# Kernel tuning notes

Measured on AMD Instinct MI355X. Metric: run time of the kernel, lower is better.

Reference implementation:

```python
import jax, jax.numpy as jnp
import numpy as np

N, S = 65536, 2048        # dense points, sampled centres
D1, D2 = 64, 256          # skip-feature dim, centre-embedding dim
MLP = [256, 128]          # conv1x1 channel stack
BN_EPS = 1e-5             # flax BatchNorm default
INTERP_EPS = 1e-8


def setup_inputs() -> dict:
    key = jax.random.key(0)
    ks = jax.random.split(key, 6)
    inp = {
        "xyz1": jax.random.normal(ks[0], (3, N), jnp.float32),
        "xyz2": jax.random.normal(ks[1], (3, S), jnp.float32),
        "points1": jax.random.normal(ks[2], (D1, N), jnp.float32),
        "points2": jax.random.normal(ks[3], (D2, S), jnp.float32),
    }
    c_in = D1 + D2
    for i, c_out in enumerate(MLP):
        inp[f"w{i}"] = jax.random.normal(ks[4 + i], (c_in, c_out), jnp.float32) / np.float32(np.sqrt(c_in))
        inp[f"b{i}"] = jnp.zeros((c_out,), jnp.float32)
        inp[f"scale{i}"] = jnp.ones((c_out,), jnp.float32)
        inp[f"bias{i}"] = jnp.zeros((c_out,), jnp.float32)
        inp[f"mean{i}"] = jnp.zeros((c_out,), jnp.float32)   # BN running mean
        inp[f"var{i}"] = jnp.ones((c_out,), jnp.float32)     # BN running var
        c_in = c_out
    return inp


def reference(xyz1, xyz2, points1, points2,
              w0, b0, scale0, bias0, mean0, var0,
              w1, b1, scale1, bias1, mean1, var1):
    x1 = xyz1.T            # [N, 3]
    x2 = xyz2.T            # [S, 3]
    p2 = points2.T         # [S, D2]

    # squared pairwise distances [N, S]
    dists = (jnp.sum(x1 * x1, -1, keepdims=True)
             + jnp.sum(x2 * x2, -1)[None, :]
             - 2.0 * (x1 @ x2.T))

    # 3 nearest neighbours (smallest dist) per dense point
    neg_d3, idx = jax.lax.top_k(-dists, 3)      # [N, 3]
    d3 = -neg_d3
    recip = 1.0 / (d3 + INTERP_EPS)
    w = recip / jnp.sum(recip, axis=1, keepdims=True)   # [N, 3]

    # inverse-distance-weighted interpolation: [N, D2]
    interp = jnp.einsum('nkd,nk->nd', p2[idx], w)

    new = jnp.concatenate([points1.T, interp], axis=-1)  # [N, D1+D2]

    # conv1x1 (== dense) + BN (inference, running stats) + ReLU stack
    for W, b, s, bb, m, v in ((w0, b0, scale0, bias0, mean0, var0),
                              (w1, b1, scale1, bias1, mean1, var1)):
        y = new @ W + b
        y = (y - m) * (s / jnp.sqrt(v + BN_EPS)) + bb
        new = jax.nn.relu(y)

    return new.T           # [MLP[-1], N]
```

## Files before the change

### kernel.cpp

```cpp
#include <hip/hip_runtime.h>
#include <math.h>

#define NPTS 65536
#define NS   2048
#define C2   256
#define C3   128

#define WS_XYZ2P   0
#define WS_P2T     32768
#define WS_W0F     1081344
#define WS_W1F     1245184
#define WS_AB0     1310720
#define WS_AB1     1312768
#define WS_KIDX    1313792
#define WS_KW      2100224

typedef __attribute__((ext_vector_type(8))) short bf16x8;
typedef __attribute__((ext_vector_type(4))) float f32x4;

__device__ __forceinline__ unsigned short f2bf(float f) {
  unsigned u = __builtin_bit_cast(unsigned, f);
  u = (u + 0x7FFFu + ((u >> 16) & 1u)) >> 16;
  return (unsigned short)u;
}
__device__ __forceinline__ float bf2f(unsigned h) {
  return __builtin_bit_cast(float, h << 16);
}

__global__ __launch_bounds__(256) void pnfp_prep(
    const float* __restrict__ points2,
    const float* __restrict__ w0, const float* __restrict__ b0,
    const float* __restrict__ scale0, const float* __restrict__ bias0,
    const float* __restrict__ mean0, const float* __restrict__ var0,
    const float* __restrict__ w1, const float* __restrict__ b1,
    const float* __restrict__ scale1, const float* __restrict__ bias1,
    const float* __restrict__ mean1, const float* __restrict__ var1,
    unsigned char* __restrict__ ws)
{
  __shared__ float tile[64][65];
  const int tid = threadIdx.x;

  if (blockIdx.x < 128) {
    const int st = blockIdx.x & 31;
    const int dt = blockIdx.x >> 5;
#pragma unroll
    for (int it = 0; it < 16; ++it) {
      int j = it * 256 + tid;
      int d = j >> 6, s = j & 63;
      tile[d][s] = points2[(dt * 64 + d) * NS + st * 64 + s];
    }
    __syncthreads();
    unsigned short* p2t = (unsigned short*)(ws + WS_P2T);
#pragma unroll
    for (int it = 0; it < 16; ++it) {
      int j = it * 256 + tid;
      int s = j >> 6, d = j & 63;
      p2t[(st * 64 + s) * 256 + dt * 64 + d] = f2bf(tile[d][s]);
    }
    return;
  }

  int gid = (blockIdx.x - 128) * 256 + tid;
  if (gid < 81920) {
    int i = gid & 7, l = (gid >> 3) & 63, c = (gid >> 9) & 15, ks = gid >> 13;
    int k = ks * 32 + (l >> 4) * 8 + i;
    int col = c * 16 + (l & 15);
    ((unsigned short*)(ws + WS_W0F))[gid] = f2bf(w0[k * C2 + col]);
    return;
  }
  gid -= 81920;
  if (gid < 32768) {
    int i = gid & 7, l = (gid >> 3) & 63, c = (gid >> 9) & 7, ks = gid >> 12;
    int k = ks * 32 + (l >> 4) * 8 + i;
    int col = c * 16 + (l & 15);
    ((unsigned short*)(ws + WS_W1F))[gid] = f2bf(w1[k * C3 + col]);
    return;
  }
  gid -= 32768;
  if (gid < 256) {
    float a = scale0[gid] / sqrtf(var0[gid] + 1e-5f);
    float bb = (b0[gid] - mean0[gid]) * a + bias0[gid];
    float* ab = (float*)(ws + WS_AB0);
    ab[gid] = a; ab[256 + gid] = bb;
    return;
  }
  gid -= 256;
  if (gid < 128) {
    float a = scale1[gid] / sqrtf(var1[gid] + 1e-5f);
    float bb = (b1[gid] - mean1[gid]) * a + bias1[gid];
    float* ab = (float*)(ws + WS_AB1);
    ab[gid] = a; ab[128 + gid] = bb;
  }
}

__global__ __launch_bounds__(256) void pnfp_knn(
    const float* __restrict__ xyz1, const float* __restrict__ xyz2,
    unsigned char* __restrict__ ws)
{
  __shared__ float4 cs[2056];
  for (int j = threadIdx.x; j < NS; j += 256) {
    float x = xyz2[j], y = xyz2[NS + j], z = xyz2[2 * NS + j];
    float sc;
    {
#pragma clang fp contract(off)
      sc = (x * x + y * y) + z * z;
    }
    cs[j + (j >> 8)] = make_float4(x, y, z, sc);
  }
  __syncthreads();

  const int tid = threadIdx.x;
  const int rank = tid & 7;
  const int set = tid >> 3;
  const int nb = blockIdx.x * 128 + set * 4;

  float px[4], py[4], pz[4], ps[4];
#pragma unroll
  for (int p = 0; p < 4; ++p) {
    int n = nb + p;
    px[p] = xyz1[n]; py[p] = xyz1[NPTS + n]; pz[p] = xyz1[2 * NPTS + n];
    {
#pragma clang fp contract(off)
      ps[p] = (px[p] * px[p] + py[p] * py[p]) + pz[p] * pz[p];
    }
  }

  float D0[4], D1[4], D2[4];
  int I0[4], I1[4], I2[4];
#pragma unroll
  for (int p = 0; p < 4; ++p) {
    D0[p] = 1e30f; D1[p] = 1e30f; D2[p] = 1e30f;
    I0[p] = 0; I1[p] = 0; I2[p] = 0;
  }

  const float4* cq = cs + rank * 257;
  const int sbase = rank << 8;
#pragma unroll 4
  for (int t = 0; t < 256; ++t) {
    const float4 c = cq[t];
    const int s = sbase + t;
#pragma unroll
    for (int p = 0; p < 4; ++p) {
      float dot = fmaf(pz[p], c.z, fmaf(py[p], c.y, px[p] * c.x));
      float d = (ps[p] + c.w) - 2.0f * dot;
      const bool c2 = d < D2[p], c1 = d < D1[p], c0 = d < D0[p];
      I2[p] = c2 ? (c1 ? I1[p] : s) : I2[p];
      I1[p] = c1 ? (c0 ? I0[p] : s) : I1[p];
      I0[p] = c0 ? s : I0[p];
      float n1 = __builtin_amdgcn_fmed3f(D0[p], D1[p], d);
      float n2 = __builtin_amdgcn_fmed3f(D1[p], D2[p], d);
      D0[p] = fminf(D0[p], d);
      D1[p] = n1; D2[p] = n2;
    }
  }

#pragma unroll
  for (int p = 0; p < 4; ++p) {
#pragma unroll
    for (int m = 1; m <= 4; m <<= 1) {
      float e0 = __shfl_xor(D0[p], m), e1 = __shfl_xor(D1[p], m), e2 = __shfl_xor(D2[p], m);
      int  j0 = __shfl_xor(I0[p], m), j1 = __shfl_xor(I1[p], m), j2 = __shfl_xor(I2[p], m);
      bool t0 = e0 < D0[p];
      float r0 = t0 ? e0 : D0[p]; int ri0 = t0 ? j0 : I0[p];
      float X0 = t0 ? D0[p] : D1[p], X1 = t0 ? D1[p] : D2[p];
      int  XI0 = t0 ? I0[p] : I1[p], XI1 = t0 ? I1[p] : I2[p];
      float Y0 = t0 ? e1 : e0, Y1v = t0 ? e2 : e1;
      int  YJ0 = t0 ? j1 : j0, YJ1 = t0 ? j2 : j1;
      bool t1 = Y0 < X0;
      float r1 = t1 ? Y0 : X0; int ri1 = t1 ? YJ0 : XI0;
      float X0b = t1 ? X0 : X1; int XI0b = t1 ? XI0 : XI1;
      float Y0b = t1 ? Y1v : Y0; int YJ0b = t1 ? YJ1 : YJ0;
      bool t2 = Y0b < X0b;
      float r2 = t2 ? Y0b : X0b; int ri2 = t2 ? YJ0b : XI0b;
      D0[p] = r0; D1[p] = r1; D2[p] = r2; I0[p] = ri0; I1[p] = ri1; I2[p] = ri2;
    }
  }

  if (rank == 0) {
#pragma unroll
    for (int p = 0; p < 4; ++p) {
      const int n = nb + p;
      float q0 = 1.0f / (D0[p] + 1e-8f);
      float q1 = 1.0f / (D1[p] + 1e-8f);
      float q2 = 1.0f / (D2[p] + 1e-8f);
      float qs = (q0 + q1) + q2;
      int* oi = (int*)(ws + WS_KIDX) + 3 * n;
      float* owp = (float*)(ws + WS_KW) + 3 * n;
      oi[0] = I0[p]; oi[1] = I1[p]; oi[2] = I2[p];
      owp[0] = q0 / qs; owp[1] = q1 / qs; owp[2] = q2 / qs;
    }
  }
}

__global__ __launch_bounds__(256, 3) void pnfp_fused(
    const float* __restrict__ points1,
    const unsigned char* __restrict__ ws,
    float* __restrict__ out)
{
  __shared__ __align__(16) unsigned char smem[41984];
  unsigned short* Fh = (unsigned short*)smem;
  const unsigned short* p2t = (const unsigned short*)(ws + WS_P2T);
  const unsigned short* w0f = (const unsigned short*)(ws + WS_W0F);
  const unsigned short* w1f = (const unsigned short*)(ws + WS_W1F);
  const float* ab0 = (const float*)(ws + WS_AB0);
  const float* ab1 = (const float*)(ws + WS_AB1);
  const int* kidx = (const int*)(ws + WS_KIDX);
  const float* kw = (const float*)(ws + WS_KW);

  const int tid = threadIdx.x;
  const int wv = tid >> 6, lane = tid & 63;
  const int n0 = blockIdx.x * 64;

#pragma unroll
  for (int it = 0; it < 16; ++it) {
    int j = tid + it * 256;
    int d = j >> 6, r = j & 63;
    Fh[r * 328 + d] = f2bf(points1[d * NPTS + n0 + r]);
  }
  {
    const int dbase = lane * 4;
#pragma unroll 2
    for (int rr = 0; rr < 16; ++rr) {
      const int r = wv * 16 + rr, n = n0 + r;
      const int a0 = kidx[3 * n], a1 = kidx[3 * n + 1], a2 = kidx[3 * n + 2];
      const float w0 = kw[3 * n], w1 = kw[3 * n + 1], w2 = kw[3 * n + 2];
      uint2 u0 = *(const uint2*)(p2t + a0 * 256 + dbase);
      uint2 u1 = *(const uint2*)(p2t + a1 * 256 + dbase);
      uint2 u2 = *(const uint2*)(p2t + a2 * 256 + dbase);
      float f0 = fmaf(w2, bf2f(u2.x & 0xFFFFu), fmaf(w1, bf2f(u1.x & 0xFFFFu), w0 * bf2f(u0.x & 0xFFFFu)));
      float f1 = fmaf(w2, bf2f(u2.x >> 16),     fmaf(w1, bf2f(u1.x >> 16),     w0 * bf2f(u0.x >> 16)));
      float f2v = fmaf(w2, bf2f(u2.y & 0xFFFFu), fmaf(w1, bf2f(u1.y & 0xFFFFu), w0 * bf2f(u0.y & 0xFFFFu)));
      float f3 = fmaf(w2, bf2f(u2.y >> 16),     fmaf(w1, bf2f(u1.y >> 16),     w0 * bf2f(u0.y >> 16)));
      uint2 pk;
      pk.x = (unsigned)f2bf(f0) | ((unsigned)f2bf(f1) << 16);
      pk.y = (unsigned)f2bf(f2v) | ((unsigned)f2bf(f3) << 16);
      *(uint2*)(Fh + r * 328 + 64 + dbase) = pk;
    }
  }
  __syncthreads();

  f32x4 zero4 = {0.f, 0.f, 0.f, 0.f};
  f32x4 acc[4][4];
#pragma unroll
  for (int a = 0; a < 4; ++a)
#pragma unroll
    for (int b = 0; b < 4; ++b) acc[a][b] = zero4;

  const int arow = lane & 15;
  const int koff = (lane >> 4) * 8;
  bf16x8 bcur[4], bnxt[4];
#pragma unroll
  for (int ct = 0; ct < 4; ++ct)
    bcur[ct] = *(const bf16x8*)(w0f + ((wv * 4 + ct) * 64 + lane) * 8);
  for (int ks = 0; ks < 10; ++ks) {
#pragma unroll
    for (int ct = 0; ct < 4; ++ct)
      bnxt[ct] = *(const bf16x8*)(w0f + (((ks + 1) * 16 + wv * 4 + ct) * 64 + lane) * 8);
    bf16x8 af[4];
#pragma unroll
    for (int rt = 0; rt < 4; ++rt)
      af[rt] = *(const bf16x8*)(Fh + (rt * 16 + arow) * 328 + ks * 32 + koff);
#pragma unroll
    for (int ct = 0; ct < 4; ++ct)
#pragma unroll
      for (int rt = 0; rt < 4; ++rt)
        acc[rt][ct] = __builtin_amdgcn_mfma_f32_16x16x32_bf16(af[rt], bcur[ct], acc[rt][ct], 0, 0, 0);
#pragma unroll
    for (int ct = 0; ct < 4; ++ct) bcur[ct] = bnxt[ct];
  }
  __syncthreads();

  unsigned short* Y1 = (unsigned short*)smem;
#pragma unroll
  for (int ct = 0; ct < 4; ++ct) {
    const int c = wv * 64 + ct * 16 + arow;
    const float a = ab0[c], b = ab0[256 + c];
#pragma unroll
    for (int rt = 0; rt < 4; ++rt) {
      const int rbase = rt * 16 + (lane >> 4) * 4;
#pragma unroll
      for (int qi = 0; qi < 4; ++qi) {
        float yv = fmaxf(fmaf(acc[rt][ct][qi], a, b), 0.0f);
        Y1[(rbase + qi) * 264 + c] = f2bf(yv);
      }
    }
  }
  __syncthreads();

  f32x4 acc2[4][2];
#pragma unroll
  for (int a = 0; a < 4; ++a) { acc2[a][0] = zero4; acc2[a][1] = zero4; }
  bf16x8 b2cur[2], b2nxt[2];
#pragma unroll
  for (int ct = 0; ct < 2; ++ct)
    b2cur[ct] = *(const bf16x8*)(w1f + ((wv * 2 + ct) * 64 + lane) * 8);
  for (int ks = 0; ks < 8; ++ks) {
#pragma unroll
    for (int ct = 0; ct < 2; ++ct)
      b2nxt[ct] = *(const bf16x8*)(w1f + (((ks + 1) * 8 + wv * 2 + ct) * 64 + lane) * 8);
    bf16x8 af[4];
#pragma unroll
    for (int rt = 0; rt < 4; ++rt)
      af[rt] = *(const bf16x8*)(Y1 + (rt * 16 + arow) * 264 + ks * 32 + koff);
#pragma unroll
    for (int ct = 0; ct < 2; ++ct)
#pragma unroll
      for (int rt = 0; rt < 4; ++rt)
        acc2[rt][ct] = __builtin_amdgcn_mfma_f32_16x16x32_bf16(af[rt], b2cur[ct], acc2[rt][ct], 0, 0, 0);
#pragma unroll
    for (int ct = 0; ct < 2; ++ct) b2cur[ct] = b2nxt[ct];
  }
  __syncthreads();

  float* OUT = (float*)smem;
#pragma unroll
  for (int ct = 0; ct < 2; ++ct) {
    const int c = wv * 32 + ct * 16 + arow;
    const float a = ab1[c], b = ab1[128 + c];
#pragma unroll
    for (int rt = 0; rt < 4; ++rt) {
      const int rbase = rt * 16 + (lane >> 4) * 4;
#pragma unroll
      for (int qi = 0; qi < 4; ++qi)
        OUT[c * 67 + rbase + qi] = fmaxf(fmaf(acc2[rt][ct][qi], a, b), 0.0f);
    }
  }
  __syncthreads();
#pragma unroll
  for (int it = 0; it < 32; ++it) {
    int j = tid + it * 256;
    int c = j >> 6, n = j & 63;
    out[c * NPTS + n0 + n] = OUT[c * 67 + n];
  }
}

extern "C" void kernel_launch(void* const* d_in, const int* in_sizes, int n_in,
                              void* d_out, int out_size, void* d_ws, size_t ws_size,
                              hipStream_t stream) {
  (void)in_sizes; (void)n_in; (void)out_size; (void)ws_size;
  const float* xyz1    = (const float*)d_in[0];
  const float* xyz2    = (const float*)d_in[1];
  const float* points1 = (const float*)d_in[2];
  const float* points2 = (const float*)d_in[3];
  const float* w0      = (const float*)d_in[4];
  const float* b0      = (const float*)d_in[5];
  const float* scale0  = (const float*)d_in[6];
  const float* bias0   = (const float*)d_in[7];
  const float* mean0   = (const float*)d_in[8];
  const float* var0    = (const float*)d_in[9];
  const float* w1      = (const float*)d_in[10];
  const float* b1      = (const float*)d_in[11];
  const float* scale1  = (const float*)d_in[12];
  const float* bias1   = (const float*)d_in[13];
  const float* mean1   = (const float*)d_in[14];
  const float* var1    = (const float*)d_in[15];
  unsigned char* ws = (unsigned char*)d_ws;
  float* out = (float*)d_out;

  pnfp_prep<<<578, 256, 0, stream>>>(points2, w0, b0, scale0, bias0, mean0, var0,
                                     w1, b1, scale1, bias1, mean1, var1, ws);
  pnfp_knn<<<512, 256, 0, stream>>>(xyz1, xyz2, ws);
  pnfp_fused<<<1024, 256, 0, stream>>>(points1, ws, out);
}
```

Before: 206.5 us.

## Merge prep into kNN launch, split centres over 16 lanes, stage kNN indices in LDS

Folds the weight/feature preparation kernel into the kNN kernel as extra blocks, removing one launch and letting prep overlap the kNN work. The kNN search now splits the 2048 centres across 16 lanes per point group instead of 8, giving 64 points per block and doubling the grid to 1024 kNN blocks, with one more shuffle-merge stage at the end. The fused MLP kernel loads each block's neighbour indices and weights into shared memory once, adding a barrier and unrolling the gather loop further. The cost is a longer merge, more blocks reloading the centre table, and slightly more LDS in the fused kernel.

```diff
diff --git a/kernel.cpp b/kernel.cpp
--- a/kernel.cpp
+++ b/kernel.cpp
@@ -6,7 +6,6 @@
 #define C2   256
 #define C3   128
 
-#define WS_XYZ2P   0
 #define WS_P2T     32768
 #define WS_W0F     1081344
 #define WS_W1F     1245184
@@ -27,7 +26,8 @@
   return __builtin_bit_cast(float, h << 16);
 }
 
-__global__ __launch_bounds__(256) void pnfp_prep(
+__global__ __launch_bounds__(256) void pnfp_knn(
+    const float* __restrict__ xyz1, const float* __restrict__ xyz2,
     const float* __restrict__ points2,
     const float* __restrict__ w0, const float* __restrict__ b0,
     const float* __restrict__ scale0, const float* __restrict__ bias0,
@@ -37,82 +37,79 @@
     const float* __restrict__ mean1, const float* __restrict__ var1,
     unsigned char* __restrict__ ws)
 {
-  __shared__ float tile[64][65];
+  __shared__ __align__(16) unsigned char kns[33024];
   const int tid = threadIdx.x;
 
-  if (blockIdx.x < 128) {
-    const int st = blockIdx.x & 31;
-    const int dt = blockIdx.x >> 5;
-#pragma unroll
-    for (int it = 0; it < 16; ++it) {
-      int j = it * 256 + tid;
-      int d = j >> 6, s = j & 63;
-      tile[d][s] = points2[(dt * 64 + d) * NS + st * 64 + s];
-    }
-    __syncthreads();
-    unsigned short* p2t = (unsigned short*)(ws + WS_P2T);
-#pragma unroll
-    for (int it = 0; it < 16; ++it) {
-      int j = it * 256 + tid;
-      int s = j >> 6, d = j & 63;
-      p2t[(st * 64 + s) * 256 + dt * 64 + d] = f2bf(tile[d][s]);
+  if (blockIdx.x >= 1024) {
+    const int pbid = blockIdx.x - 1024;
+    if (pbid < 128) {
+      float (*tile)[65] = (float(*)[65])kns;
+      const int st = pbid & 31, dt = pbid >> 5;
+#pragma unroll
+      for (int it = 0; it < 16; ++it) {
+        int j = it * 256 + tid;
+        int d = j >> 6, s = j & 63;
+        tile[d][s] = points2[(dt * 64 + d) * NS + st * 64 + s];
+      }
+      __syncthreads();
+      unsigned short* p2t = (unsigned short*)(ws + WS_P2T);
+#pragma unroll
+      for (int it = 0; it < 16; ++it) {
+        int j = it * 256 + tid;
+        int s = j >> 6, d = j & 63;
+        p2t[(st * 64 + s) * 256 + dt * 64 + d] = f2bf(tile[d][s]);
+      }
+      return;
+    }
+    int gid = (pbid - 128) * 256 + tid;
+    if (gid < 81920) {
+      int i = gid & 7, l = (gid >> 3) & 63, c = (gid >> 9) & 15, ks = gid >> 13;
+      int k = ks * 32 + (l >> 4) * 8 + i;
+      int col = c * 16 + (l & 15);
+      ((unsigned short*)(ws + WS_W0F))[gid] = f2bf(w0[k * C2 + col]);
+      return;
+    }
+    gid -= 81920;
+    if (gid < 32768) {
+      int i = gid & 7, l = (gid >> 3) & 63, c = (gid >> 9) & 7, ks = gid >> 12;
+      int k = ks * 32 + (l >> 4) * 8 + i;
+      int col = c * 16 + (l & 15);
+      ((unsigned short*)(ws + WS_W1F))[gid] = f2bf(w1[k * C3 + col]);
+      return;
+    }
+    gid -= 32768;
+    if (gid < 256) {
+      float a = scale0[gid] / sqrtf(var0[gid] + 1e-5f);
+      float bb = (b0[gid] - mean0[gid]) * a + bias0[gid];
+      float* ab = (float*)(ws + WS_AB0);
+      ab[gid] = a; ab[256 + gid] = bb;
+      return;
+    }
+    gid -= 256;
+    if (gid < 128) {
+      float a = scale1[gid] / sqrtf(var1[gid] + 1e-5f);
+      float bb = (b1[gid] - mean1[gid]) * a + bias1[gid];
+      float* ab = (float*)(ws + WS_AB1);
+      ab[gid] = a; ab[128 + gid] = bb;
     }
     return;
   }
 
-  int gid = (blockIdx.x - 128) * 256 + tid;
-  if (gid < 81920) {
-    int i = gid & 7, l = (gid >> 3) & 63, c = (gid >> 9) & 15, ks = gid >> 13;
-    int k = ks * 32 + (l >> 4) * 8 + i;
-    int col = c * 16 + (l & 15);
-    ((unsigned short*)(ws + WS_W0F))[gid] = f2bf(w0[k * C2 + col]);
-    return;
-  }
-  gid -= 81920;
-  if (gid < 32768) {
-    int i = gid & 7, l = (gid >> 3) & 63, c = (gid >> 9) & 7, ks = gid >> 12;
-    int k = ks * 32 + (l >> 4) * 8 + i;
-    int col = c * 16 + (l & 15);
-    ((unsigned short*)(ws + WS_W1F))[gid] = f2bf(w1[k * C3 + col]);
-    return;
-  }
-  gid -= 32768;
-  if (gid < 256) {
-    float a = scale0[gid] / sqrtf(var0[gid] + 1e-5f);
-    float bb = (b0[gid] - mean0[gid]) * a + bias0[gid];
-    float* ab = (float*)(ws + WS_AB0);
-    ab[gid] = a; ab[256 + gid] = bb;
-    return;
-  }
-  gid -= 256;
-  if (gid < 128) {
-    float a = scale1[gid] / sqrtf(var1[gid] + 1e-5f);
-    float bb = (b1[gid] - mean1[gid]) * a + bias1[gid];
-    float* ab = (float*)(ws + WS_AB1);
-    ab[gid] = a; ab[128 + gid] = bb;
-  }
-}
-
-__global__ __launch_bounds__(256) void pnfp_knn(
-    const float* __restrict__ xyz1, const float* __restrict__ xyz2,
-    unsigned char* __restrict__ ws)
-{
-  __shared__ float4 cs[2056];
-  for (int j = threadIdx.x; j < NS; j += 256) {
+  float4* cs = (float4*)kns;
+  for (int j = tid; j < NS; j += 256) {
     float x = xyz2[j], y = xyz2[NS + j], z = xyz2[2 * NS + j];
     float sc;
     {
 #pragma clang fp contract(off)
       sc = (x * x + y * y) + z * z;
     }
-    cs[j + (j >> 8)] = make_float4(x, y, z, sc);
-  }
-  __syncthreads();
-
-  const int tid = threadIdx.x;
-  const int rank = tid & 7;
-  const int set = tid >> 3;
-  const int nb = blockIdx.x * 128 + set * 4;
+    cs[(j >> 7) * 129 + (j & 127)] = make_float4(x, y, z, sc);
+  }
+  __syncthreads();
+
+  const int rank = tid & 15;
+  const int set = tid >> 4;
+  const int nb = blockIdx.x * 64 + set * 4;
 
   float px[4], py[4], pz[4], ps[4];
 #pragma unroll
@@ -133,10 +130,10 @@
     I0[p] = 0; I1[p] = 0; I2[p] = 0;
   }
 
-  const float4* cq = cs + rank * 257;
-  const int sbase = rank << 8;
+  const float4* cq = cs + rank * 129;
+  const int sbase = rank << 7;
 #pragma unroll 4
-  for (int t = 0; t < 256; ++t) {
+  for (int t = 0; t < 128; ++t) {
     const float4 c = cq[t];
     const int s = sbase + t;
 #pragma unroll
@@ -157,7 +154,7 @@
 #pragma unroll
   for (int p = 0; p < 4; ++p) {
 #pragma unroll
-    for (int m = 1; m <= 4; m <<= 1) {
+    for (int m = 1; m <= 8; m <<= 1) {
       float e0 = __shfl_xor(D0[p], m), e1 = __shfl_xor(D1[p], m), e2 = __shfl_xor(D2[p], m);
       int  j0 = __shfl_xor(I0[p], m), j1 = __shfl_xor(I1[p], m), j2 = __shfl_xor(I2[p], m);
       bool t0 = e0 < D0[p];
@@ -197,8 +194,10 @@
     const unsigned char* __restrict__ ws,
     float* __restrict__ out)
 {
-  __shared__ __align__(16) unsigned char smem[41984];
+  __shared__ __align__(16) unsigned char smem[43520];
   unsigned short* Fh = (unsigned short*)smem;
+  int*   kI = (int*)(smem + 41984);
+  float* kW = (float*)(smem + 42752);
   const unsigned short* p2t = (const unsigned short*)(ws + WS_P2T);
   const unsigned short* w0f = (const unsigned short*)(ws + WS_W0F);
   const unsigned short* w1f = (const unsigned short*)(ws + WS_W1F);
@@ -211,19 +210,24 @@
   const int wv = tid >> 6, lane = tid & 63;
   const int n0 = blockIdx.x * 64;
 
+  if (tid < 192) {
+    kI[tid] = kidx[3 * n0 + tid];
+    kW[tid] = kw[3 * n0 + tid];
+  }
 #pragma unroll
   for (int it = 0; it < 16; ++it) {
     int j = tid + it * 256;
     int d = j >> 6, r = j & 63;
     Fh[r * 328 + d] = f2bf(points1[d * NPTS + n0 + r]);
   }
+  __syncthreads();
   {
     const int dbase = lane * 4;
-#pragma unroll 2
+#pragma unroll 4
     for (int rr = 0; rr < 16; ++rr) {
-      const int r = wv * 16 + rr, n = n0 + r;
-      const int a0 = kidx[3 * n], a1 = kidx[3 * n + 1], a2 = kidx[3 * n + 2];
-      const float w0 = kw[3 * n], w1 = kw[3 * n + 1], w2 = kw[3 * n + 2];
+      const int r = wv * 16 + rr;
+      const int a0 = kI[3 * r], a1 = kI[3 * r + 1], a2 = kI[3 * r + 2];
+      const float w0 = kW[3 * r], w1 = kW[3 * r + 1], w2 = kW[3 * r + 2];
       uint2 u0 = *(const uint2*)(p2t + a0 * 256 + dbase);
       uint2 u1 = *(const uint2*)(p2t + a1 * 256 + dbase);
       uint2 u2 = *(const uint2*)(p2t + a2 * 256 + dbase);
@@ -357,8 +361,8 @@
   unsigned char* ws = (unsigned char*)d_ws;
   float* out = (float*)d_out;
 
-  pnfp_prep<<<578, 256, 0, stream>>>(points2, w0, b0, scale0, bias0, mean0, var0,
+  pnfp_knn<<<1602, 256, 0, stream>>>(xyz1, xyz2, points2,
+                                     w0, b0, scale0, bias0, mean0, var0,
                                      w1, b1, scale1, bias1, mean1, var1, ws);
-  pnfp_knn<<<512, 256, 0, stream>>>(xyz1, xyz2, ws);
   pnfp_fused<<<1024, 256, 0, stream>>>(points1, ws, out);
 }
```

After: 204.9 us. No clear change (-0.8%).
